# Optimization experiments

Measured on AMD Instinct MI355X. Metric: run time of the kernel, lower is better.

Reference implementation:

```python
import jax, jax.numpy as jnp
import numpy as np

# dims
N, T, M, V = 64, 64, 2, 25
CIN, COUT = 64, 128
K, STRIDE, PAD = 3, 1, 1
EMB_H = 64  # Embed hidden width
BN_EPS = 1e-5


def conv1d(x, w, b, stride, pad):
    # x: (B, C, T), w: (O, I, K), b: (O,)
    y = jax.lax.conv_general_dilated(
        x, w, window_strides=(stride,), padding=[(pad, pad)],
        dimension_numbers=('NCH', 'OIH', 'NCH'))
    return y + b[None, :, None]


def setup_inputs() -> dict:
    key = jax.random.key(0)
    ks = jax.random.split(key, 20)
    f32 = jnp.float32
    inp = {
        'x': jax.random.normal(ks[0], (N, T, M, V, CIN), f32),
        'G': jax.random.uniform(ks[1], (N, T, M, V, V), f32) * 0.2,
        # embed_joint: Linear(V,64)+ReLU, Linear(64,CIN)+ReLU
        'ej_w1': jax.random.normal(ks[2], (V, EMB_H), f32) * 0.1,
        'ej_b1': jnp.zeros((EMB_H,), f32),
        'ej_w2': jax.random.normal(ks[3], (EMB_H, CIN), f32) * 0.1,
        'ej_b2': jnp.zeros((CIN,), f32),
        # embed_frame: Linear(T,64)+ReLU, Linear(64,COUT)+ReLU
        'ef_w1': jax.random.normal(ks[4], (T, EMB_H), f32) * 0.1,
        'ef_b1': jnp.zeros((EMB_H,), f32),
        'ef_w2': jax.random.normal(ks[5], (EMB_H, COUT), f32) * 0.1,
        'ef_b2': jnp.zeros((COUT,), f32),
        # GCN: h = relu((adj @ x) @ W + b)
        'gcn_w': jax.random.normal(ks[6], (2 * CIN, COUT), f32) * 0.05,
        'gcn_b': jnp.zeros((COUT,), f32),
        # tcn: Conv1d(COUT,COUT,K) + BN(eval) + ReLU
        'tcn_w': jax.random.normal(ks[7], (COUT, COUT, K), f32) * 0.05,
        'tcn_b': jnp.zeros((COUT,), f32),
        'bn_gamma': jnp.ones((COUT,), f32),
        'bn_beta': jnp.zeros((COUT,), f32),
        'bn_mean': jax.random.normal(ks[8], (COUT,), f32) * 0.01,
        'bn_var': jnp.ones((COUT,), f32),
        # adj_tcn: Conv1d(V,V,K)
        'adj_w': jax.random.normal(ks[9], (V, V, K), f32) * 0.05,
        'adj_b': jnp.zeros((V,), f32),
    }
    return inp


def reference(x, G, ej_w1, ej_b1, ej_w2, ej_b2, ef_w1, ef_b1, ef_w2, ef_b2,
              gcn_w, gcn_b, tcn_w, tcn_b, bn_gamma, bn_beta, bn_mean, bn_var,
              adj_w, adj_b):
    n, t, m, v, c = x.shape
    # embed_joint(one_hot(V)): one-hot @ W1 == W1, so the MLP acts on rows
    ej = jax.nn.relu(jax.nn.relu(ej_w1 + ej_b1) @ ej_w2 + ej_b2)  # (V, CIN)
    xcat = jnp.concatenate([x, jnp.broadcast_to(ej, (n, t, m, v, c))], axis=-1)  # (N,T,M,V,2C)
    # batched dense GCN over N*T*M small VxV graphs
    adjx = jnp.einsum('ntmuv,ntmvc->ntmuc', G, xcat)
    h = jax.nn.relu(adjx @ gcn_w + gcn_b)  # (N,T,M,V,COUT)
    # embed_frame(one_hot(T)) added with broadcast over (N,M,V)
    ef = jax.nn.relu(jax.nn.relu(ef_w1 + ef_b1) @ ef_w2 + ef_b2)  # (T, COUT)
    h = h + ef[None, :, None, None, :]
    cout = h.shape[-1]
    hx = h.transpose(0, 2, 3, 4, 1).reshape(n * m * v, cout, t)
    gx = G.transpose(0, 2, 3, 4, 1).reshape(n * m * v, v, t)
    y = conv1d(hx, tcn_w, tcn_b, STRIDE, PAD)
    y = (y - bn_mean[None, :, None]) * jax.lax.rsqrt(bn_var + BN_EPS)[None, :, None]
    y = jax.nn.relu(y * bn_gamma[None, :, None] + bn_beta[None, :, None])
    gy = conv1d(gx, adj_w, adj_b, STRIDE, PAD)
    t_out = y.shape[-1]
    x_out = y.reshape(n, m, v, cout, t_out).transpose(0, 4, 1, 2, 3)
    g_out = gy.reshape(n, m, v, v, t_out).transpose(0, 4, 1, 2, 3)
    return (x_out, g_out)
```

## Files before the change

kernel.cpp:

```cpp
#include <hip/hip_runtime.h>

#define NN 64
#define TT 64
#define MM 2
#define VV 25
#define CI 64
#define CO 128
#define EMBH 64

typedef __attribute__((ext_vector_type(8))) short short8;
typedef __attribute__((ext_vector_type(4))) float f32x4;

#define WS_EJW 0
#define WS_EF  3200
#define WS_S   11392
#define WS_BC  11520
#define WS_CT  11648
#define WS_WH  19840
#define WS_WL  44416
#define WS_HHI 68992
#define WS_HLO 13176192
#define XOUT_ELEMS 26214400

__device__ __forceinline__ unsigned short bf16_rne(float f) {
  unsigned u = __float_as_uint(f);
  unsigned r = u + 0x7FFFu + ((u >> 16) & 1u);
  return (unsigned short)(r >> 16);
}
__device__ __forceinline__ float bf16_to_f(unsigned short h) {
  return __uint_as_float((unsigned)h << 16);
}

__global__ void k0a_ej(const float* __restrict__ ej_w1, const float* __restrict__ ej_b1,
                       const float* __restrict__ ej_w2, const float* __restrict__ ej_b2,
                       const float* __restrict__ gcn_w, const float* __restrict__ tcn_b,
                       const float* __restrict__ bn_gamma, const float* __restrict__ bn_beta,
                       const float* __restrict__ bn_mean, const float* __restrict__ bn_var,
                       float* __restrict__ ws) {
  __shared__ float tmp1[VV * EMBH];
  __shared__ float ejs[VV * EMBH];
  int tid = threadIdx.x;
  for (int i = tid; i < VV * EMBH; i += 256)
    tmp1[i] = fmaxf(ej_w1[i] + ej_b1[i & 63], 0.f);
  __syncthreads();
  for (int i = tid; i < VV * EMBH; i += 256) {
    int v = i >> 6, c = i & 63;
    float a = ej_b2[c];
    for (int h = 0; h < EMBH; ++h) a = fmaf(tmp1[v * EMBH + h], ej_w2[h * CI + c], a);
    ejs[i] = fmaxf(a, 0.f);
  }
  __syncthreads();
  for (int i = tid; i < VV * CO; i += 256) {
    int v = i >> 7, o = i & 127;
    float a = 0.f;
    for (int c = 0; c < CI; ++c) a = fmaf(ejs[v * EMBH + c], gcn_w[(CI + c) * CO + o], a);
    ws[WS_EJW + i] = a;
  }
  if (tid < CO) {
    float s = bn_gamma[tid] * rsqrtf(bn_var[tid] + 1e-5f);
    ws[WS_S + tid] = s;
    ws[WS_BC + tid] = tcn_b[tid] * s + bn_beta[tid] - bn_mean[tid] * s;
  }
}

__global__ void k0b_ef(const float* __restrict__ ef_w1, const float* __restrict__ ef_b1,
                       const float* __restrict__ ef_w2, const float* __restrict__ ef_b2,
                       float* __restrict__ ws) {
  __shared__ float tf[EMBH];
  int t = blockIdx.x, o = threadIdx.x;
  if (o < EMBH) tf[o] = fmaxf(ef_w1[t * EMBH + o] + ef_b1[o], 0.f);
  __syncthreads();
  float a = ef_b2[o];
#pragma unroll
  for (int h = 0; h < EMBH; ++h) a = fmaf(tf[h], ef_w2[h * CO + o], a);
  ws[WS_EF + t * CO + o] = fmaxf(a, 0.f);
}

__global__ void k_wt2(const float* __restrict__ tcn_w, float* __restrict__ ws) {
  int j = blockIdx.x * 256 + threadIdx.x;
  if (j >= 3 * CO * CO) return;
  int s = j >> 14, rr = j & 16383, o = rr >> 7, c = rr & 127;
  float f = tcn_w[o * (CO * 3) + c * 3 + s];
  unsigned short hi = bf16_rne(f);
  float lo = f - bf16_to_f(hi);
  ((unsigned short*)(ws + WS_WH))[j] = hi;
  ((unsigned short*)(ws + WS_WL))[j] = bf16_rne(lo);
}

__global__ void k1_ct(const float* __restrict__ tcn_w, const float* __restrict__ ws_ro,
                      float* __restrict__ ct_out) {
  __shared__ float ef3[3 * CO];
  int t = blockIdx.x, o = threadIdx.x;
  for (int i = o; i < 3 * CO; i += 128) {
    int k = i >> 7, c = i & 127, tt = t + k - 1;
    ef3[i] = (tt >= 0 && tt < TT) ? ws_ro[WS_EF + tt * CO + c] : 0.f;
  }
  __syncthreads();
  const float* wp = tcn_w + o * (CO * 3);
  float a = 0.f;
  for (int c = 0; c < CO; ++c) {
    a = fmaf(ef3[c], wp[c * 3 + 0], a);
    a = fmaf(ef3[CO + c], wp[c * 3 + 1], a);
    a = fmaf(ef3[2 * CO + c], wp[c * 3 + 2], a);
  }
  ct_out[t * CO + o] = fmaf(a, ws_ro[WS_S + o], ws_ro[WS_BC + o]);
}

__global__ void __launch_bounds__(256, 4) k_gcn(const float* __restrict__ x, const float* __restrict__ G,
                                                const float* __restrict__ gcn_w, const float* __restrict__ gcn_b,
                                                const float* __restrict__ ejW, float* __restrict__ ws) {
  __shared__ float xs[VV * CI];
  __shared__ float Gs[VV * VV];
  __shared__ float Ps[2][VV * CO];
  int ntm = blockIdx.x;
  int tid = threadIdx.x;
  const float* xb = x + (size_t)ntm * (VV * CI);
  for (int i = tid; i < VV * CI; i += 256) xs[i] = xb[i];
  const float* Gb = G + (size_t)ntm * (VV * VV);
  for (int i = tid; i < VV * VV; i += 256) Gs[i] = Gb[i];
  int o = tid & 127, h = tid >> 7;
  float wreg[32];
#pragma unroll
  for (int c = 0; c < 32; ++c) wreg[c] = gcn_w[(h * 32 + c) * CO + o];
  __syncthreads();
  for (int v = 0; v < VV; ++v) {
    float a = h ? 0.f : ejW[v * CO + o];
    const float4* xv = (const float4*)&xs[v * CI + h * 32];
#pragma unroll
    for (int c4 = 0; c4 < 8; ++c4) {
      float4 q = xv[c4];
      a = fmaf(q.x, wreg[4 * c4 + 0], a);
      a = fmaf(q.y, wreg[4 * c4 + 1], a);
      a = fmaf(q.z, wreg[4 * c4 + 2], a);
      a = fmaf(q.w, wreg[4 * c4 + 3], a);
    }
    Ps[h][v * CO + o] = a;
  }
  __syncthreads();
  float psum[VV];
#pragma unroll
  for (int v = 0; v < VV; ++v) psum[v] = Ps[0][v * CO + o] + Ps[1][v * CO + o];
  float bo = gcn_b[o];
  unsigned short* hh_g = (unsigned short*)(ws + WS_HHI);
  unsigned short* hl_g = (unsigned short*)(ws + WS_HLO);
  size_t base = (size_t)ntm * (VV * CO);
  for (int u = h; u < VV; u += 2) {
    float a = bo;
#pragma unroll
    for (int v = 0; v < VV; ++v) a = fmaf(Gs[u * VV + v], psum[v], a);
    float y = fmaxf(a, 0.f);
    unsigned short hi = bf16_rne(y);
    float lo = y - bf16_to_f(hi);
    hh_g[base + u * CO + o] = hi;
    hl_g[base + u * CO + o] = bf16_rne(lo);
  }
}

__global__ void __launch_bounds__(512) k_tcn(const float* __restrict__ ws_ro,
                                             float* __restrict__ out) {
  __shared__ __align__(16) unsigned short h2[2 * 68 * 128];
  int b = blockIdx.x;
  int n = b / (MM * VV), r = b % (MM * VV), m = r / VV, v = r % VV;
  int tid = threadIdx.x;
  const unsigned short* hh_g = (const unsigned short*)(ws_ro + WS_HHI);
  const unsigned short* hl_g = (const unsigned short*)(ws_ro + WS_HLO);
  size_t gbase = ((size_t)(n * TT * MM + m) * VV + v) * CO;
#pragma unroll
  for (int arr = 0; arr < 2; ++arr) {
    const unsigned short* src = arr ? hl_g : hh_g;
#pragma unroll
    for (int rep = 0; rep < 2; ++rep) {
      int task = rep * 512 + tid;
      int t = task >> 4, chunk = task & 15;
      int row = t + 1;
      int4 val = *(const int4*)(src + gbase + (size_t)t * (MM * VV * CO) + chunk * 8);
      int elem = arr * 8704 + row * 128 + ((((chunk * 16) ^ ((row & 7) << 4))) >> 1);
      *(int4*)(&h2[elem]) = val;
    }
  }
  if (tid < 64) {
    int arr = tid >> 5, rr = (tid >> 4) & 1, chunk = tid & 15;
    int row = rr ? 65 : 0;
    int elem = arr * 8704 + row * 128 + ((((chunk * 16) ^ ((row & 7) << 4))) >> 1);
    int4 z = {0, 0, 0, 0};
    *(int4*)(&h2[elem]) = z;
  }
  __syncthreads();
  int w = tid >> 6, l = tid & 63;
  int o0 = w * 16, lm = l & 15, lg = l >> 4;
  const unsigned short* wh_g = (const unsigned short*)(ws_ro + WS_WH);
  const unsigned short* wl_g = (const unsigned short*)(ws_ro + WS_WL);
  short8 bh[3][4], bl[3][4];
#pragma unroll
  for (int s = 0; s < 3; ++s)
#pragma unroll
    for (int ks = 0; ks < 4; ++ks) {
      int idx = (s * CO + o0 + lm) * CO + ks * 32 + lg * 8;
      bh[s][ks] = *(const short8*)(wh_g + idx);
      bl[s][ks] = *(const short8*)(wl_g + idx);
    }
  float so = ws_ro[WS_S + o0 + lm];
  float* ob = out + gbase;
  for (int tq = 0; tq < 4; ++tq) {
    f32x4 ahh = {0.f, 0.f, 0.f, 0.f}, alh = {0.f, 0.f, 0.f, 0.f}, ahl = {0.f, 0.f, 0.f, 0.f};
#pragma unroll
    for (int s = 0; s < 3; ++s) {
      int row = tq * 16 + lm + s;
      int rbase = row * 128, sw = (row & 7) << 4;
#pragma unroll
      for (int ks = 0; ks < 4; ++ks) {
        int eo = rbase + (((ks * 64 + lg * 16) ^ sw) >> 1);
        short8 Ah = *(const short8*)(&h2[eo]);
        short8 Al = *(const short8*)(&h2[8704 + eo]);
        ahh = __builtin_amdgcn_mfma_f32_16x16x32_bf16(Ah, bh[s][ks], ahh, 0, 0, 0);
        alh = __builtin_amdgcn_mfma_f32_16x16x32_bf16(Al, bh[s][ks], alh, 0, 0, 0);
        ahl = __builtin_amdgcn_mfma_f32_16x16x32_bf16(Ah, bl[s][ks], ahl, 0, 0, 0);
      }
    }
#pragma unroll
    for (int rr = 0; rr < 4; ++rr) {
      int t = tq * 16 + lg * 4 + rr;
      float acc = ahh[rr] + alh[rr] + ahl[rr];
      float y = fmaxf(fmaf(acc, so, ws_ro[WS_CT + t * CO + o0 + lm]), 0.f);
      ob[(size_t)t * (MM * VV * CO) + o0 + lm] = y;
    }
  }
}

__global__ void k_adj(const float* __restrict__ G, const float* __restrict__ adj_w,
                      const float* __restrict__ adj_b, float* __restrict__ gout) {
  __shared__ float Gs3[3 * VV * VV];
  __shared__ float wls[VV * VV * 3];
  int ntm = blockIdx.x;
  int n = ntm / (TT * MM), r = ntm % (TT * MM), t = r / MM, m = r % MM;
  int tid = threadIdx.x;
  for (int i = tid; i < 3 * VV * VV; i += 256) {
    int k = i / (VV * VV), e = i % (VV * VV), tt = t + k - 1;
    Gs3[i] = (tt >= 0 && tt < TT) ? G[((size_t)((n * TT + tt) * MM + m)) * (VV * VV) + e] : 0.f;
  }
  for (int i = tid; i < VV * VV * 3; i += 256) wls[i] = adj_w[i];
  __syncthreads();
  for (int e = tid; e < VV * VV; e += 256) {
    int u = e / VV, o = e % VV;
    float a = adj_b[o];
#pragma unroll
    for (int i = 0; i < VV; ++i) {
      a = fmaf(Gs3[u * VV + i], wls[o * 75 + i * 3 + 0], a);
      a = fmaf(Gs3[VV * VV + u * VV + i], wls[o * 75 + i * 3 + 1], a);
      a = fmaf(Gs3[2 * VV * VV + u * VV + i], wls[o * 75 + i * 3 + 2], a);
    }
    gout[(size_t)ntm * (VV * VV) + e] = a;
  }
}

extern "C" void kernel_launch(void* const* d_in, const int* in_sizes, int n_in,
                              void* d_out, int out_size, void* d_ws, size_t ws_size,
                              hipStream_t stream) {
  const float* x     = (const float*)d_in[0];
  const float* G     = (const float*)d_in[1];
  const float* ej_w1 = (const float*)d_in[2];
  const float* ej_b1 = (const float*)d_in[3];
  const float* ej_w2 = (const float*)d_in[4];
  const float* ej_b2 = (const float*)d_in[5];
  const float* ef_w1 = (const float*)d_in[6];
  const float* ef_b1 = (const float*)d_in[7];
  const float* ef_w2 = (const float*)d_in[8];
  const float* ef_b2 = (const float*)d_in[9];
  const float* gcn_w = (const float*)d_in[10];
  const float* gcn_b = (const float*)d_in[11];
  const float* tcn_w = (const float*)d_in[12];
  const float* tcn_b = (const float*)d_in[13];
  const float* bn_g  = (const float*)d_in[14];
  const float* bn_b  = (const float*)d_in[15];
  const float* bn_m  = (const float*)d_in[16];
  const float* bn_v  = (const float*)d_in[17];
  const float* adj_w = (const float*)d_in[18];
  const float* adj_b = (const float*)d_in[19];
  float* out = (float*)d_out;
  float* ws  = (float*)d_ws;

  k0a_ej<<<1, 256, 0, stream>>>(ej_w1, ej_b1, ej_w2, ej_b2, gcn_w, tcn_b, bn_g, bn_b, bn_m, bn_v, ws);
  k0b_ef<<<TT, CO, 0, stream>>>(ef_w1, ef_b1, ef_w2, ef_b2, ws);
  k_wt2<<<(3 * CO * CO + 255) / 256, 256, 0, stream>>>(tcn_w, ws);
  k1_ct<<<TT, CO, 0, stream>>>(tcn_w, ws, ws + WS_CT);
  k_gcn<<<NN * TT * MM, 256, 0, stream>>>(x, G, gcn_w, gcn_b, ws + WS_EJW, ws);
  k_tcn<<<NN * MM * VV, 512, 0, stream>>>(ws, out);
  k_adj<<<NN * TT * MM, 256, 0, stream>>>(G, adj_w, adj_b, out + XOUT_ELEMS);
}
```

Measured before the change: 518.4 us.

## Move GCN matmuls onto bf16 MFMA with hi/lo split precision

Rewrites the GCN kernel so both products, x@W and G@P, run on 16x16x32 bf16 MFMA instructions instead of scalar FMAs. Each operand is split into bf16 hi and lo parts and three MFMAs are combined to keep near-fp32 accuracy. A new small kernel pre-splits and transposes gcn_w into a workspace region that reuses the space of the no-longer-needed frame-embedding buffer. This adds conversion work, zero-padding of V=25 to 32, and swizzled shared-memory layouts, in exchange for removing the scalar FMA bottleneck.

```diff
diff --git a/kernel.cpp b/kernel.cpp
--- a/kernel.cpp
+++ b/kernel.cpp
@@ -13,6 +13,8 @@
 
 #define WS_EJW 0
 #define WS_EF  3200
+#define WS_WGH 3200
+#define WS_WGL 7296
 #define WS_S   11392
 #define WS_BC  11520
 #define WS_CT  11648
@@ -87,6 +89,17 @@
   ((unsigned short*)(ws + WS_WL))[j] = bf16_rne(lo);
 }
 
+__global__ void k_wg(const float* __restrict__ gcn_w, float* __restrict__ ws) {
+  int j = blockIdx.x * 256 + threadIdx.x;
+  if (j >= CO * CI) return;
+  int o = j >> 6, c = j & 63;
+  float f = gcn_w[c * CO + o];
+  unsigned short hi = bf16_rne(f);
+  float lo = f - bf16_to_f(hi);
+  ((unsigned short*)(ws + WS_WGH))[j] = hi;
+  ((unsigned short*)(ws + WS_WGL))[j] = bf16_rne(lo);
+}
+
 __global__ void k1_ct(const float* __restrict__ tcn_w, const float* __restrict__ ws_ro,
                       float* __restrict__ ct_out) {
   __shared__ float ef3[3 * CO];
@@ -107,52 +120,126 @@
 }
 
 __global__ void __launch_bounds__(256, 4) k_gcn(const float* __restrict__ x, const float* __restrict__ G,
-                                                const float* __restrict__ gcn_w, const float* __restrict__ gcn_b,
-                                                const float* __restrict__ ejW, float* __restrict__ ws) {
-  __shared__ float xs[VV * CI];
-  __shared__ float Gs[VV * VV];
-  __shared__ float Ps[2][VV * CO];
+                                                const float* __restrict__ gcn_b, float* __restrict__ ws) {
+  __shared__ __align__(16) unsigned short xh[32 * 64], xl[32 * 64];
+  __shared__ __align__(16) unsigned short Gh[32 * 40], Gl[32 * 40];
+  __shared__ __align__(16) unsigned short Ph[128 * 40], Pl[128 * 40];
   int ntm = blockIdx.x;
   int tid = threadIdx.x;
+  int w = tid >> 6, l = tid & 63, lm = l & 15, lg = l >> 4;
+  int o0 = w * 32;
+
+  const unsigned short* wgh = (const unsigned short*)(ws + WS_WGH);
+  const unsigned short* wgl = (const unsigned short*)(ws + WS_WGL);
+  short8 wfh[2][2], wfl[2][2];
+#pragma unroll
+  for (int nt = 0; nt < 2; ++nt)
+#pragma unroll
+    for (int ks = 0; ks < 2; ++ks) {
+      int idx = (o0 + nt * 16 + lm) * CI + ks * 32 + lg * 8;
+      wfh[nt][ks] = *(const short8*)(wgh + idx);
+      wfl[nt][ks] = *(const short8*)(wgl + idx);
+    }
+
+  {
+    unsigned* xh32 = (unsigned*)xh; unsigned* xl32 = (unsigned*)xl;
+    for (int i = tid; i < 1024; i += 256) { xh32[i] = 0u; xl32[i] = 0u; }
+    unsigned* gh32 = (unsigned*)Gh; unsigned* gl32 = (unsigned*)Gl;
+    for (int i = tid; i < 640; i += 256) { gh32[i] = 0u; gl32[i] = 0u; }
+  }
+  __syncthreads();
   const float* xb = x + (size_t)ntm * (VV * CI);
-  for (int i = tid; i < VV * CI; i += 256) xs[i] = xb[i];
+  for (int i = tid; i < VV * CI; i += 256) {
+    int v = i >> 6, c = i & 63;
+    float f = xb[i];
+    unsigned short hi = bf16_rne(f);
+    float lo = f - bf16_to_f(hi);
+    int elem = v * 64 + (((c * 2) ^ ((v & 7) << 4)) >> 1);
+    xh[elem] = hi;
+    xl[elem] = bf16_rne(lo);
+  }
   const float* Gb = G + (size_t)ntm * (VV * VV);
-  for (int i = tid; i < VV * VV; i += 256) Gs[i] = Gb[i];
-  int o = tid & 127, h = tid >> 7;
-  float wreg[32];
-#pragma unroll
-  for (int c = 0; c < 32; ++c) wreg[c] = gcn_w[(h * 32 + c) * CO + o];
-  __syncthreads();
-  for (int v = 0; v < VV; ++v) {
-    float a = h ? 0.f : ejW[v * CO + o];
-    const float4* xv = (const float4*)&xs[v * CI + h * 32];
-#pragma unroll
-    for (int c4 = 0; c4 < 8; ++c4) {
-      float4 q = xv[c4];
-      a = fmaf(q.x, wreg[4 * c4 + 0], a);
-      a = fmaf(q.y, wreg[4 * c4 + 1], a);
-      a = fmaf(q.z, wreg[4 * c4 + 2], a);
-      a = fmaf(q.w, wreg[4 * c4 + 3], a);
-    }
-    Ps[h][v * CO + o] = a;
-  }
-  __syncthreads();
-  float psum[VV];
-#pragma unroll
-  for (int v = 0; v < VV; ++v) psum[v] = Ps[0][v * CO + o] + Ps[1][v * CO + o];
-  float bo = gcn_b[o];
+  for (int i = tid; i < VV * VV; i += 256) {
+    int u = i / VV, vc = i - u * VV;
+    float f = Gb[i];
+    unsigned short hi = bf16_rne(f);
+    float lo = f - bf16_to_f(hi);
+    Gh[u * 40 + vc] = hi;
+    Gl[u * 40 + vc] = bf16_rne(lo);
+  }
+  __syncthreads();
+
+  const float* ejW = ws + WS_EJW;
+#pragma unroll
+  for (int mt = 0; mt < 2; ++mt) {
+#pragma unroll
+    for (int nt = 0; nt < 2; ++nt) {
+      f32x4 hh = {0.f, 0.f, 0.f, 0.f}, lh = {0.f, 0.f, 0.f, 0.f}, hl = {0.f, 0.f, 0.f, 0.f};
+      int row = mt * 16 + lm, rbase = row * 128, sw = (row & 7) << 4;
+#pragma unroll
+      for (int ks = 0; ks < 2; ++ks) {
+        int eo = (rbase + (((ks * 64 + lg * 16) ^ sw))) >> 1;
+        short8 Ah = *(const short8*)(&xh[eo]);
+        short8 Al = *(const short8*)(&xl[eo]);
+        hh = __builtin_amdgcn_mfma_f32_16x16x32_bf16(Ah, wfh[nt][ks], hh, 0, 0, 0);
+        lh = __builtin_amdgcn_mfma_f32_16x16x32_bf16(Al, wfh[nt][ks], lh, 0, 0, 0);
+        hl = __builtin_amdgcn_mfma_f32_16x16x32_bf16(Ah, wfl[nt][ks], hl, 0, 0, 0);
+      }
+      int o = o0 + nt * 16 + lm;
+      int vb = mt * 16 + lg * 4;
+      unsigned short ph[4], pl[4];
+#pragma unroll
+      for (int r = 0; r < 4; ++r) {
+        int v = vb + r;
+        float e = (v < VV) ? ejW[v * CO + o] : 0.f;
+        float acc = hh[r] + lh[r] + hl[r] + e;
+        unsigned short hi = bf16_rne(acc);
+        float lo = acc - bf16_to_f(hi);
+        ph[r] = hi;
+        pl[r] = bf16_rne(lo);
+      }
+      uint2 hv, lv;
+      hv.x = (unsigned)ph[0] | ((unsigned)ph[1] << 16);
+      hv.y = (unsigned)ph[2] | ((unsigned)ph[3] << 16);
+      lv.x = (unsigned)pl[0] | ((unsigned)pl[1] << 16);
+      lv.y = (unsigned)pl[2] | ((unsigned)pl[3] << 16);
+      *(uint2*)(&Ph[o * 40 + vb]) = hv;
+      *(uint2*)(&Pl[o * 40 + vb]) = lv;
+    }
+  }
+  __syncthreads();
+
   unsigned short* hh_g = (unsigned short*)(ws + WS_HHI);
   unsigned short* hl_g = (unsigned short*)(ws + WS_HLO);
   size_t base = (size_t)ntm * (VV * CO);
-  for (int u = h; u < VV; u += 2) {
-    float a = bo;
-#pragma unroll
-    for (int v = 0; v < VV; ++v) a = fmaf(Gs[u * VV + v], psum[v], a);
-    float y = fmaxf(a, 0.f);
-    unsigned short hi = bf16_rne(y);
-    float lo = y - bf16_to_f(hi);
-    hh_g[base + u * CO + o] = hi;
-    hl_g[base + u * CO + o] = bf16_rne(lo);
+#pragma unroll
+  for (int mt = 0; mt < 2; ++mt) {
+#pragma unroll
+    for (int nt = 0; nt < 2; ++nt) {
+      f32x4 hh = {0.f, 0.f, 0.f, 0.f}, lh = {0.f, 0.f, 0.f, 0.f}, hl = {0.f, 0.f, 0.f, 0.f};
+      int ga = (mt * 16 + lm) * 40 + lg * 8;
+      int pa = (o0 + nt * 16 + lm) * 40 + lg * 8;
+      short8 Ah = *(const short8*)(&Gh[ga]);
+      short8 Al = *(const short8*)(&Gl[ga]);
+      short8 Bh = *(const short8*)(&Ph[pa]);
+      short8 Bl = *(const short8*)(&Pl[pa]);
+      hh = __builtin_amdgcn_mfma_f32_16x16x32_bf16(Ah, Bh, hh, 0, 0, 0);
+      lh = __builtin_amdgcn_mfma_f32_16x16x32_bf16(Al, Bh, lh, 0, 0, 0);
+      hl = __builtin_amdgcn_mfma_f32_16x16x32_bf16(Ah, Bl, hl, 0, 0, 0);
+      int o = o0 + nt * 16 + lm;
+      float bo = gcn_b[o];
+#pragma unroll
+      for (int r = 0; r < 4; ++r) {
+        int u = mt * 16 + lg * 4 + r;
+        if (u < VV) {
+          float y = fmaxf(hh[r] + lh[r] + hl[r] + bo, 0.f);
+          unsigned short hi = bf16_rne(y);
+          float lo = y - bf16_to_f(hi);
+          hh_g[base + u * CO + o] = hi;
+          hl_g[base + u * CO + o] = bf16_rne(lo);
+        }
+      }
+    }
   }
 }
 
@@ -283,7 +370,8 @@
   k0b_ef<<<TT, CO, 0, stream>>>(ef_w1, ef_b1, ef_w2, ef_b2, ws);
   k_wt2<<<(3 * CO * CO + 255) / 256, 256, 0, stream>>>(tcn_w, ws);
   k1_ct<<<TT, CO, 0, stream>>>(tcn_w, ws, ws + WS_CT);
-  k_gcn<<<NN * TT * MM, 256, 0, stream>>>(x, G, gcn_w, gcn_b, ws + WS_EJW, ws);
+  k_wg<<<(CO * CI + 255) / 256, 256, 0, stream>>>(gcn_w, ws);
+  k_gcn<<<NN * TT * MM, 256, 0, stream>>>(x, G, gcn_b, ws);
   k_tcn<<<NN * MM * VV, 512, 0, stream>>>(ws, out);
   k_adj<<<NN * TT * MM, 256, 0, stream>>>(G, adj_w, adj_b, out + XOUT_ELEMS);
 }
```

Result: faster. 475.6 us (-8.3%).
